# Performance work log

Hardware: AMD Instinct MI355X
Metric: run time of the kernel (lower is better)

The kernel has to match this reference:

```python
import jax, jax.numpy as jnp
import numpy as np

D = 32          # d_lat // 2
D_ANCIL = 16
HID = 128
GRID = 64
N = GRID * GRID # n_patch / n_state
B = 8
DT = 0.25
T_MAX = 4.0
N_STEPS = 18    # enough half/full Strang steps to exceed T_MAX for all batch elems


def _grid_neighbours(g):
    # 4 nearest neighbours on a periodic g x g dual mesh
    idx = np.arange(g * g).reshape(g, g)
    nbrs = np.stack([np.roll(idx, 1, 0), np.roll(idx, -1, 0),
                     np.roll(idx, 1, 1), np.roll(idx, -1, 1)], axis=-1)
    return jnp.asarray(nbrs.reshape(g * g, 4), dtype=jnp.int32)


def setup_inputs() -> dict:
    key = jax.random.key(0)
    ks = jax.random.split(key, 8)
    din = 2 * D + D_ANCIL  # concat(z, neighbour-mean z, xi)
    s1 = 1.0 / np.sqrt(din)
    s2 = 1.0 / np.sqrt(HID)
    return {
        "x": jax.random.normal(ks[0], (B, N, 2 * D + D_ANCIL), jnp.float32),
        "t_final": jax.random.uniform(ks[1], (B,), jnp.float32) * T_MAX,
        "W1_q": jax.random.normal(ks[2], (din, HID), jnp.float32) * s1,
        "b1_q": jnp.zeros((HID,), jnp.float32),
        "W2_q": jax.random.normal(ks[3], (HID, D), jnp.float32) * s2,
        "b2_q": jnp.zeros((D,), jnp.float32),
        "W1_p": jax.random.normal(ks[4], (din, HID), jnp.float32) * s1,
        "b1_p": jnp.zeros((HID,), jnp.float32),
        "W2_p": jax.random.normal(ks[5], (HID, D), jnp.float32) * s2,
        "b2_p": jnp.zeros((D,), jnp.float32),
        "nbrs": _grid_neighbours(GRID),
    }


def _F(z, xi, nbrs, W1, b1, W2, b2):
    # nearest-neighbour forcing: per-node MLP on (z, mean of neighbour z, xi)
    z_nbr = jnp.mean(z[:, nbrs, :], axis=2)           # (B,N,4,D) -> (B,N,D)
    h = jnp.tanh(jnp.concatenate([z, z_nbr, xi], axis=-1) @ W1 + b1)
    return h @ W2 + b2                                 # (B,N,D)


def _masked_stepsize(t, t_final, dt):
    # per-batch stepsize, clipped so integration stops exactly at t_final
    return jnp.clip(t_final - t, 0.0, dt)


def reference(x, t_final, W1_q, b1_q, W2_q, b2_q, W1_p, b1_p, W2_p, b2_p, nbrs):
    q = x[..., :D]
    p = x[..., D:2 * D]
    xi = x[..., 2 * D:]
    tf = t_final[:, None, None]  # broadcast over (N, D)

    def step(carry, k):
        q, p, t_q, t_p = carry
        rho = jnp.where(k == 0, jnp.float32(0.5), jnp.float32(1.0))
        dt_q = _masked_stepsize(t_q, tf, rho * DT)
        q = q + dt_q * _F(p, xi, nbrs, W1_q, b1_q, W2_q, b2_q)
        t_q = t_q + rho * DT
        dt_p = _masked_stepsize(t_p, tf, DT)
        p = p + dt_p * _F(q, xi, nbrs, W1_p, b1_p, W2_p, b2_p)
        t_p = t_p + DT
        return (q, p, t_q, t_p), None

    init = (q, p, jnp.float32(0.0), jnp.float32(0.0))
    (q, p, _, _), _ = jax.lax.scan(step, init, jnp.arange(N_STEPS))
    return jnp.concatenate([q, p, xi], axis=-1)
```

## Files before the change

kernel.cpp:

```cpp
#include <hip/hip_runtime.h>
#include <hip/hip_bf16.h>

#define GRID_W 64
#define NPTS   4096
#define BATCH  8
#define DD     32
#define DIN    80
#define HID    128
#define SH_STRIDE 136
#define SQ_STRIDE 36
#define NBLK   512
#define NSTEP  34
#define OFF_F1Q 131072
#define OFF_F2Q (OFF_F1Q + 24*64*16)
#define OFF_F1P (OFF_F2Q + 8*64*16)
#define OFF_F2P (OFF_F1P + 24*64*16)
#define OFF_EBUF 262144

typedef __attribute__((ext_vector_type(8))) short short8;
typedef __attribute__((ext_vector_type(4))) float f32x4;
typedef unsigned long long u64;

__device__ __forceinline__ ushort f2bf(float v) {
    __hip_bfloat16 h = __float2bfloat16(v);
    return __builtin_bit_cast(ushort, h);
}
__device__ __forceinline__ uint packbf(float a, float b) {
    return (uint)f2bf(a) | ((uint)f2bf(b) << 16);
}
__device__ __forceinline__ short8 pack8(float4 a, float4 b) {
    union { uint u[4]; short8 s; } t;
    t.u[0] = packbf(a.x, a.y); t.u[1] = packbf(a.z, a.w);
    t.u[2] = packbf(b.x, b.y); t.u[3] = packbf(b.z, b.w);
    return t.s;
}
__device__ __forceinline__ float bf2f(ushort u) {
    union { uint i; float f; } t; t.i = ((uint)u) << 16; return t.f;
}

__device__ __forceinline__ short8 ld_sysh8(const ushort* p) {
    union { u64 v[2]; short8 s; } t;
    t.v[0] = __hip_atomic_load((const u64*)p,       __ATOMIC_RELAXED, __HIP_MEMORY_SCOPE_SYSTEM);
    t.v[1] = __hip_atomic_load((const u64*)(p + 4), __ATOMIC_RELAXED, __HIP_MEMORY_SCOPE_SYSTEM);
    return t.s;
}
__device__ __forceinline__ void st_sysb4(ushort* p, float4 v) {
    u64 pk = (u64)packbf(v.x, v.y) | ((u64)packbf(v.z, v.w) << 32);
    __hip_atomic_store((u64*)p, pk, __ATOMIC_RELAXED, __HIP_MEMORY_SCOPE_SYSTEM);
}

__global__ void setup_all(const float* __restrict__ x, float* __restrict__ out,
                          char* __restrict__ ws,
                          const float* __restrict__ W1q, const float* __restrict__ W2q,
                          const float* __restrict__ W1p, const float* __restrict__ W2p)
{
    const int blk = blockIdx.x, tid = threadIdx.x;
    if (blk >= NBLK) {
        const int s = blk - NBLK;
        const float* W1 = s ? W1p : W1q;
        const float* W2 = s ? W2p : W2q;
        ushort* f1 = (ushort*)(ws + (s ? OFF_F1P : OFF_F1Q));
        ushort* f2 = (ushort*)(ws + (s ? OFF_F2P : OFF_F2Q));
        for (int idx = tid; idx < 24 * 512; idx += 256) {
            int f = idx >> 9, rem = idx & 511, lane = rem >> 3, j = rem & 7;
            int ks = f >> 3, nt = f & 7;
            int k = ks * 32 + (lane >> 4) * 8 + j, n = nt * 16 + (lane & 15);
            f1[idx] = f2bf(k < DIN ? W1[k * HID + n] : 0.0f);
        }
        for (int idx = tid; idx < 8 * 512; idx += 256) {
            int f = idx >> 9, rem = idx & 511, lane = rem >> 3, j = rem & 7;
            int ks = f >> 1, nt = f & 1;
            int k = ks * 32 + (lane >> 4) * 8 + j, n = nt * 16 + (lane & 15);
            f2[idx] = f2bf(W2[k * DD + n]);
        }
        return;
    }
    const int b = blk >> 6, r = blk & 63;
    if (tid < 64) ((uint*)ws)[blk * 64 + tid] = 0u;
    const int pt = tid >> 2, j4 = tid & 3;
    {
        const float* src = x   + (size_t)(b * NPTS + r * GRID_W + pt) * DIN + j4 * 20;
        float*       dst = out + (size_t)(b * NPTS + r * GRID_W + pt) * DIN + j4 * 20;
        #pragma unroll
        for (int i = 0; i < 5; ++i)
            *(float4*)(dst + i * 4) = *(const float4*)(src + i * 4);
    }
    {
        const int sg = j4 * 8;
        const float* src = x + (size_t)(b * NPTS + r * GRID_W + pt) * DIN;
        ushort* drow = (ushort*)(ws + OFF_EBUF) + ((size_t)(b * 64 + r) * 64 + pt) * 64;
        float4 q0 = *(const float4*)(src + sg),      q1 = *(const float4*)(src + sg + 4);
        float4 p0 = *(const float4*)(src + DD + sg), p1 = *(const float4*)(src + DD + sg + 4);
        *(uint*)&drow[sg]          = packbf(q0.x, q0.y);
        *(uint*)&drow[sg + 2]      = packbf(q0.z, q0.w);
        *(uint*)&drow[sg + 4]      = packbf(q1.x, q1.y);
        *(uint*)&drow[sg + 6]      = packbf(q1.z, q1.w);
        *(uint*)&drow[32 + sg]     = packbf(p0.x, p0.y);
        *(uint*)&drow[32 + sg + 2] = packbf(p0.z, p0.w);
        *(uint*)&drow[32 + sg + 4] = packbf(p1.x, p1.y);
        *(uint*)&drow[32 + sg + 6] = packbf(p1.z, p1.w);
    }
}

struct Acc2 { f32x4 a0, a1; };

__device__ __forceinline__ Acc2 eval_F(short8 af0, short8 af1, short8 af2,
    const short8* __restrict__ F1, const short8* __restrict__ w2,
    const float* __restrict__ B1, ushort* __restrict__ sH,
    int wv, int lane, int l16, int quad, int q8)
{
    f32x4 acc1[8];
    #pragma unroll
    for (int nt = 0; nt < 8; ++nt) acc1[nt] = (f32x4){0.f, 0.f, 0.f, 0.f};
    #pragma unroll
    for (int nt = 0; nt < 8; ++nt)
        acc1[nt] = __builtin_amdgcn_mfma_f32_16x16x32_bf16(af0, F1[nt * 64 + lane], acc1[nt], 0, 0, 0);
    #pragma unroll
    for (int nt = 0; nt < 8; ++nt)
        acc1[nt] = __builtin_amdgcn_mfma_f32_16x16x32_bf16(af1, F1[(8 + nt) * 64 + lane], acc1[nt], 0, 0, 0);
    #pragma unroll
    for (int nt = 0; nt < 8; ++nt)
        acc1[nt] = __builtin_amdgcn_mfma_f32_16x16x32_bf16(af2, F1[(16 + nt) * 64 + lane], acc1[nt], 0, 0, 0);
    #pragma unroll
    for (int nt = 0; nt < 8; ++nt) {
        const int col = nt * 16 + l16;
        const float bias = B1[col];
        #pragma unroll
        for (int rg = 0; rg < 4; ++rg) {
            const int rowm = wv * 16 + quad * 4 + rg;
            float s = acc1[nt][rg] + bias;
            float e = __expf(2.0f * s);
            float hh = 1.0f - __fdividef(2.0f, e + 1.0f);
            sH[rowm * SH_STRIDE + col] = f2bf(hh);
        }
    }
    Acc2 o;
    o.a0 = (f32x4){0.f, 0.f, 0.f, 0.f};
    o.a1 = (f32x4){0.f, 0.f, 0.f, 0.f};
    #pragma unroll
    for (int ks = 0; ks < 4; ++ks) {
        short8 af = *(const short8*)&sH[(wv * 16 + l16) * SH_STRIDE + ks * 32 + q8];
        o.a0 = __builtin_amdgcn_mfma_f32_16x16x32_bf16(af, w2[ks * 2 + 0], o.a0, 0, 0, 0);
        o.a1 = __builtin_amdgcn_mfma_f32_16x16x32_bf16(af, w2[ks * 2 + 1], o.a1, 0, 0, 0);
    }
    return o;
}

__global__ __launch_bounds__(256, 2) void sympl_coop(
    float* __restrict__ out, const float* __restrict__ tfinal,
    char* __restrict__ ws,
    const float* __restrict__ b1q, const float* __restrict__ b2q,
    const float* __restrict__ b1p, const float* __restrict__ b2p)
{
    __shared__ __align__(16) float  sQ[64 * SQ_STRIDE];
    __shared__ __align__(16) float  sP[64 * SQ_STRIDE];
    __shared__ __align__(16) ushort sH[64 * SH_STRIDE];
    __shared__ __align__(16) float  sO[4 * 512];
    __shared__ uint ldsF[4];

    uint* flags = (uint*)ws;
    ushort* ebuf = (ushort*)(ws + OFF_EBUF);
    const int blk = blockIdx.x, tid = threadIdx.x;
    const int b = blk >> 6, r = blk & 63;
    const int wv = tid >> 6, lane = tid & 63;
    const int l16 = lane & 15, quad = lane >> 4, q8 = quad * 8;
    const int c = wv * 16 + l16;
    const int rm = (r + 63) & 63, rp = (r + 1) & 63;
    const int cm = (c + 63) & 63, cp = (c + 1) & 63;
    const int pt = tid >> 2, sg = (tid & 3) * 8;

    uint* flLw = flags + (((size_t)(b * 64 + rm) * 4) + wv) * 16;
    uint* flRw = flags + (((size_t)(b * 64 + rp) * 4) + wv) * 16;
    uint* flOw = flags + (((size_t)(b * 64 + r ) * 4) + wv) * 16;

    {
        const float* src = out + (size_t)(b * NPTS + r * GRID_W + pt) * DIN;
        *(float4*)&sQ[pt * SQ_STRIDE + sg]     = *(const float4*)(src + sg);
        *(float4*)&sQ[pt * SQ_STRIDE + sg + 4] = *(const float4*)(src + sg + 4);
        *(float4*)&sP[pt * SQ_STRIDE + sg]     = *(const float4*)(src + DD + sg);
        *(float4*)&sP[pt * SQ_STRIDE + sg + 4] = *(const float4*)(src + DD + sg + 4);
    }
    if (tid < 4) ldsF[tid] = 0;
    short8 af2;
    if (quad < 2) {
        const float* px = out + (size_t)(b * NPTS + r * GRID_W + c) * DIN + 2 * DD + q8;
        af2 = pack8(*(const float4*)px, *(const float4*)(px + 4));
    } else {
        af2 = (short8)(short)0;
    }
    short8 w2q[8], w2p[8];
    {
        const short8* F2q = (const short8*)(ws + OFF_F2Q);
        const short8* F2p = (const short8*)(ws + OFF_F2P);
        #pragma unroll
        for (int i = 0; i < 8; ++i) { w2q[i] = F2q[i * 64 + lane]; w2p[i] = F2p[i * 64 + lane]; }
    }
    const float tf = tfinal[b];
    __syncthreads();

    const ushort* e_rm = ebuf + ((size_t)(b * 64 + rm) * 64 + c) * 64;
    const ushort* e_rp = ebuf + ((size_t)(b * 64 + rp) * 64 + c) * 64;
    const int wl = (wv + 3) & 3, wr = (wv + 1) & 3;

    float tq = 0.0f, tp = 0.0f;
    #pragma unroll 1
    for (int h = 0; h < NSTEP; ++h) {
        const int phase = h & 1;
        const float dtmax = phase ? 0.25f : ((h == 0) ? 0.125f : 0.25f);
        const float tcur  = phase ? tp : tq;
        if (!phase && tq >= tf) break;
        if (h > 0) {
            const uint tgt = (uint)h;
            while (true) {
                uint v = tgt;
                if (lane == 0)      v = __hip_atomic_load(flLw, __ATOMIC_RELAXED, __HIP_MEMORY_SCOPE_SYSTEM);
                else if (lane == 1) v = __hip_atomic_load(flRw, __ATOMIC_RELAXED, __HIP_MEMORY_SCOPE_SYSTEM);
                else if (lane == 2) v = __hip_atomic_load(&ldsF[wl], __ATOMIC_RELAXED, __HIP_MEMORY_SCOPE_WORKGROUP);
                else if (lane == 3) v = __hip_atomic_load(&ldsF[wr], __ATOMIC_RELAXED, __HIP_MEMORY_SCOPE_WORKGROUP);
                if (__all((int)(v >= tgt))) break;
                __builtin_amdgcn_s_sleep(1);
            }
        }

        const float dt = fminf(fmaxf(tf - tcur, 0.0f), dtmax);
        if (dt > 0.0f) {
            const int so  = phase ? 0 : 32;
            const int dso = phase ? 32 : 0;
            const float* srcL = phase ? sQ : sP;
            float*       dstL = phase ? sP : sQ;

            short8 upv = ld_sysh8(e_rm + so + q8);
            short8 dnv = ld_sysh8(e_rp + so + q8);

            const float* s0p = srcL + c * SQ_STRIDE + q8;
            float4 a0 = *(const float4*)s0p, a1 = *(const float4*)(s0p + 4);
            short8 af0 = pack8(a0, a1);

            const short8* F1 = (const short8*)(ws + (phase ? OFF_F1P : OFF_F1Q));
            f32x4 acc1[8];
            #pragma unroll
            for (int nt = 0; nt < 8; ++nt) acc1[nt] = (f32x4){0.f, 0.f, 0.f, 0.f};
            #pragma unroll
            for (int nt = 0; nt < 8; ++nt)
                acc1[nt] = __builtin_amdgcn_mfma_f32_16x16x32_bf16(af0, F1[nt * 64 + lane], acc1[nt], 0, 0, 0);
            #pragma unroll
            for (int nt = 0; nt < 8; ++nt)
                acc1[nt] = __builtin_amdgcn_mfma_f32_16x16x32_bf16(af2, F1[(16 + nt) * 64 + lane], acc1[nt], 0, 0, 0);

            const float* smp = srcL + cm * SQ_STRIDE + q8;
            const float* spp = srcL + cp * SQ_STRIDE + q8;
            float4 lf0 = *(const float4*)smp, lf1 = *(const float4*)(smp + 4);
            float4 rt0 = *(const float4*)spp, rt1 = *(const float4*)(spp + 4);
            float4 m0, m1;
            m0.x = 0.25f * (bf2f((ushort)upv[0]) + bf2f((ushort)dnv[0]) + lf0.x + rt0.x);
            m0.y = 0.25f * (bf2f((ushort)upv[1]) + bf2f((ushort)dnv[1]) + lf0.y + rt0.y);
            m0.z = 0.25f * (bf2f((ushort)upv[2]) + bf2f((ushort)dnv[2]) + lf0.z + rt0.z);
            m0.w = 0.25f * (bf2f((ushort)upv[3]) + bf2f((ushort)dnv[3]) + lf0.w + rt0.w);
            m1.x = 0.25f * (bf2f((ushort)upv[4]) + bf2f((ushort)dnv[4]) + lf1.x + rt1.x);
            m1.y = 0.25f * (bf2f((ushort)upv[5]) + bf2f((ushort)dnv[5]) + lf1.y + rt1.y);
            m1.z = 0.25f * (bf2f((ushort)upv[6]) + bf2f((ushort)dnv[6]) + lf1.z + rt1.z);
            m1.w = 0.25f * (bf2f((ushort)upv[7]) + bf2f((ushort)dnv[7]) + lf1.w + rt1.w);
            short8 af1 = pack8(m0, m1);
            #pragma unroll
            for (int nt = 0; nt < 8; ++nt)
                acc1[nt] = __builtin_amdgcn_mfma_f32_16x16x32_bf16(af1, F1[(8 + nt) * 64 + lane], acc1[nt], 0, 0, 0);

            const float* B1 = phase ? b1p : b1q;
            #pragma unroll
            for (int nt = 0; nt < 8; ++nt) {
                const int col = nt * 16 + l16;
                const float bias = B1[col];
                #pragma unroll
                for (int rg = 0; rg < 4; ++rg) {
                    const int rowm = wv * 16 + quad * 4 + rg;
                    float s = acc1[nt][rg] + bias;
                    float e = __expf(2.0f * s);
                    float hh = 1.0f - __fdividef(2.0f, e + 1.0f);
                    sH[rowm * SH_STRIDE + col] = f2bf(hh);
                }
            }
            const short8* w2 = phase ? w2p : w2q;
            f32x4 o0 = (f32x4){0.f, 0.f, 0.f, 0.f};
            f32x4 o1 = (f32x4){0.f, 0.f, 0.f, 0.f};
            #pragma unroll
            for (int ks = 0; ks < 4; ++ks) {
                short8 af = *(const short8*)&sH[(wv * 16 + l16) * SH_STRIDE + ks * 32 + q8];
                o0 = __builtin_amdgcn_mfma_f32_16x16x32_bf16(af, w2[ks * 2 + 0], o0, 0, 0, 0);
                o1 = __builtin_amdgcn_mfma_f32_16x16x32_bf16(af, w2[ks * 2 + 1], o1, 0, 0, 0);
            }
            float* sOw = sO + wv * 512;
            const float* B2 = phase ? b2p : b2q;
            #pragma unroll
            for (int nt = 0; nt < 2; ++nt) {
                const int col = nt * 16 + l16;
                const float b2v = B2[col];
                const f32x4 av = nt ? o1 : o0;
                #pragma unroll
                for (int rg = 0; rg < 4; ++rg)
                    sOw[(quad * 4 + rg) * DD + col] = av[rg] + b2v;
            }
            #pragma unroll
            for (int it = 0; it < 2; ++it) {
                const int slot = lane + it * 64;
                const int lr = slot >> 3, seg = (slot & 7) * 4;
                const int pt_ = wv * 16 + lr;
                const float* po = &sOw[lr * DD + seg];
                float* pl = dstL + pt_ * SQ_STRIDE + seg;
                float4 o = *(const float4*)pl;
                o.x += dt * po[0]; o.y += dt * po[1];
                o.z += dt * po[2]; o.w += dt * po[3];
                st_sysb4(ebuf + ((size_t)(b * 64 + r) * 64 + pt_) * 64 + dso + seg, o);
                *(float4*)pl = o;
            }
        }
        __asm__ volatile("s_waitcnt vmcnt(0)" ::: "memory");
        if (lane == 0)
            __hip_atomic_store(flOw, (uint)(h + 1), __ATOMIC_RELAXED, __HIP_MEMORY_SCOPE_SYSTEM);
        __asm__ volatile("s_waitcnt lgkmcnt(0)" ::: "memory");
        if (lane == 0)
            __hip_atomic_store(&ldsF[wv], (uint)(h + 1), __ATOMIC_RELAXED, __HIP_MEMORY_SCOPE_WORKGROUP);
        if (phase) tp += dtmax; else tq += dtmax;
    }

    {
        float* dst = out + (size_t)(b * NPTS + r * GRID_W + pt) * DIN;
        *(float4*)(dst + sg)          = *(const float4*)&sQ[pt * SQ_STRIDE + sg];
        *(float4*)(dst + sg + 4)      = *(const float4*)&sQ[pt * SQ_STRIDE + sg + 4];
        *(float4*)(dst + DD + sg)     = *(const float4*)&sP[pt * SQ_STRIDE + sg];
        *(float4*)(dst + DD + sg + 4) = *(const float4*)&sP[pt * SQ_STRIDE + sg + 4];
    }
}

__global__ __launch_bounds__(256, 2) void sympl_step(
    float* __restrict__ state, const float* __restrict__ tfinal,
    const char* __restrict__ ws,
    const float* __restrict__ B1, const float* __restrict__ B2,
    int phase, float tcur, float dtmax)
{
    __shared__ __align__(16) ushort sH[64 * SH_STRIDE];
    __shared__ __align__(16) float  sO[4 * 512];
    const int blk = blockIdx.x, tid = threadIdx.x;
    const int wv = tid >> 6, lane = tid & 63;
    const int l16 = lane & 15, quad = lane >> 4, q8 = quad * 8;
    const int b = blk >> 6, r = blk & 63;
    const int c = wv * 16 + l16;

    const float tf = tfinal[b];
    const float dt = fminf(fmaxf(tf - tcur, 0.0f), dtmax);
    if (dt <= 0.0f) return;

    const int srcoff = phase ? 0 : DD;
    const int dstoff = phase ? DD : 0;
    float* bb = state + (size_t)b * NPTS * DIN;
    const float* selfp = bb + (r * GRID_W + c) * DIN;
    const int rm = (r + 63) & 63, rp = (r + 1) & 63;
    const int cm = (c + 63) & 63, cp = (c + 1) & 63;
    short8 af0, af1, af2;
    {
        const float* ps = selfp + srcoff + q8;
        af0 = pack8(*(const float4*)ps, *(const float4*)(ps + 4));
    }
    {
        const float* p0 = bb + (rm * GRID_W + c) * DIN + srcoff + q8;
        const float* p1 = bb + (rp * GRID_W + c) * DIN + srcoff + q8;
        const float* p2 = bb + (r * GRID_W + cm) * DIN + srcoff + q8;
        const float* p3 = bb + (r * GRID_W + cp) * DIN + srcoff + q8;
        float4 a0 = *(const float4*)p0, a1 = *(const float4*)(p0 + 4);
        float4 b0 = *(const float4*)p1, b1v = *(const float4*)(p1 + 4);
        float4 c0 = *(const float4*)p2, c1 = *(const float4*)(p2 + 4);
        float4 d0 = *(const float4*)p3, d1 = *(const float4*)(p3 + 4);
        float4 m0, m1;
        m0.x = 0.25f * (a0.x + b0.x + c0.x + d0.x);
        m0.y = 0.25f * (a0.y + b0.y + c0.y + d0.y);
        m0.z = 0.25f * (a0.z + b0.z + c0.z + d0.z);
        m0.w = 0.25f * (a0.w + b0.w + c0.w + d0.w);
        m1.x = 0.25f * (a1.x + b1v.x + c1.x + d1.x);
        m1.y = 0.25f * (a1.y + b1v.y + c1.y + d1.y);
        m1.z = 0.25f * (a1.z + b1v.z + c1.z + d1.z);
        m1.w = 0.25f * (a1.w + b1v.w + c1.w + d1.w);
        af1 = pack8(m0, m1);
    }
    if (quad < 2) {
        const float* px = selfp + 2 * DD + q8;
        af2 = pack8(*(const float4*)px, *(const float4*)(px + 4));
    } else {
        af2 = (short8)(short)0;
    }
    const short8* F1 = (const short8*)(ws + (phase ? OFF_F1P : OFF_F1Q));
    const short8* F2 = (const short8*)(ws + (phase ? OFF_F2P : OFF_F2Q));
    short8 w2[8];
    #pragma unroll
    for (int i = 0; i < 8; ++i) w2[i] = F2[i * 64 + lane];
    Acc2 A = eval_F(af0, af1, af2, F1, w2, B1, sH, wv, lane, l16, quad, q8);
    float* sOw = sO + wv * 512;
    #pragma unroll
    for (int nt = 0; nt < 2; ++nt) {
        const int col = nt * 16 + l16;
        const float b2v = B2[col];
        const f32x4 av = nt ? A.a1 : A.a0;
        #pragma unroll
        for (int rg = 0; rg < 4; ++rg)
            sOw[(quad * 4 + rg) * DD + col] = av[rg] + b2v;
    }
    #pragma unroll
    for (int it = 0; it < 2; ++it) {
        const int slot = lane + it * 64;
        const int lr = slot >> 3, seg = (slot & 7) * 4;
        float* pd = bb + (r * GRID_W + wv * 16 + lr) * DIN + dstoff + seg;
        const float* po = &sOw[lr * DD + seg];
        float4 o = *(const float4*)pd;
        o.x += dt * po[0]; o.y += dt * po[1];
        o.z += dt * po[2]; o.w += dt * po[3];
        *(float4*)pd = o;
    }
}

extern "C" void kernel_launch(void* const* d_in, const int* in_sizes, int n_in,
                              void* d_out, int out_size, void* d_ws, size_t ws_size,
                              hipStream_t stream)
{
    const float* x   = (const float*)d_in[0];
    const float* tf  = (const float*)d_in[1];
    const float* W1q = (const float*)d_in[2];
    const float* b1q = (const float*)d_in[3];
    const float* W2q = (const float*)d_in[4];
    const float* b2q = (const float*)d_in[5];
    const float* W1p = (const float*)d_in[6];
    const float* b1p = (const float*)d_in[7];
    const float* W2p = (const float*)d_in[8];
    const float* b2p = (const float*)d_in[9];
    float* out = (float*)d_out;
    char* ws = (char*)d_ws;

    setup_all<<<dim3(NBLK + 2), dim3(256), 0, stream>>>(x, out, ws, W1q, W2q, W1p, W2p);

    void* args[] = { (void*)&out, (void*)&tf, (void*)&ws,
                     (void*)&b1q, (void*)&b2q, (void*)&b1p, (void*)&b2p };
    hipError_t e = hipLaunchCooperativeKernel((const void*)sympl_coop,
                                              dim3(NBLK), dim3(256), args, 0, stream);
    if (e != hipSuccess) {
        float tq = 0.0f, tp = 0.0f;
        for (int h = 0; h < NSTEP; ++h) {
            const int phase = h & 1;
            const float dtmax = phase ? 0.25f : ((h == 0) ? 0.125f : 0.25f);
            const float tcur  = phase ? tp : tq;
            sympl_step<<<dim3(NBLK), dim3(256), 0, stream>>>(
                out, tf, ws, phase ? b1p : b1q, phase ? b2p : b2q,
                phase, tcur, dtmax);
            if (phase) tp += dtmax; else tq += dtmax;
        }
    }
}
```

Baseline: 250.0 us.

## Embed step tags in halo data words and overlap first GEMM with neighbour wait

Replaces the separate per-wave flag counters with a 16-bit step tag packed into the top of every 64-bit halo word (three bf16 values plus tag), so consumers poll the data itself rather than a flag followed by a data load. The self-and-xi part of the first GEMM is moved ahead of the neighbour wait so it can overlap with the synchronisation latency. This removes the vmcnt drain and flag store on the producer side. In exchange the halo buffer grows, each consumer spins on six system-scope loads, and a workspace-size check is added before using the cooperative path.

```diff
diff --git a/kernel.cpp b/kernel.cpp
--- a/kernel.cpp
+++ b/kernel.cpp
@@ -16,6 +16,8 @@
 #define OFF_F1P (OFF_F2Q + 8*64*16)
 #define OFF_F2P (OFF_F1P + 24*64*16)
 #define OFF_EBUF 262144
+#define EB_U64_TOTAL ((size_t)NBLK * 64 * 24)
+#define WS_NEED ((size_t)OFF_EBUF + EB_U64_TOTAL * 8)
 
 typedef __attribute__((ext_vector_type(8))) short short8;
 typedef __attribute__((ext_vector_type(4))) float f32x4;
@@ -38,21 +40,18 @@
     union { uint i; float f; } t; t.i = ((uint)u) << 16; return t.f;
 }
 
-__device__ __forceinline__ short8 ld_sysh8(const ushort* p) {
-    union { u64 v[2]; short8 s; } t;
-    t.v[0] = __hip_atomic_load((const u64*)p,       __ATOMIC_RELAXED, __HIP_MEMORY_SCOPE_SYSTEM);
-    t.v[1] = __hip_atomic_load((const u64*)(p + 4), __ATOMIC_RELAXED, __HIP_MEMORY_SCOPE_SYSTEM);
-    return t.s;
-}
-__device__ __forceinline__ void st_sysb4(ushort* p, float4 v) {
-    u64 pk = (u64)packbf(v.x, v.y) | ((u64)packbf(v.z, v.w) << 32);
-    __hip_atomic_store((u64*)p, pk, __ATOMIC_RELAXED, __HIP_MEMORY_SCOPE_SYSTEM);
+__device__ __forceinline__ u64 ld_sys64(const u64* p) {
+    return __hip_atomic_load(p, __ATOMIC_RELAXED, __HIP_MEMORY_SCOPE_SYSTEM);
+}
+__device__ __forceinline__ void st_sys64(u64* p, u64 v) {
+    __hip_atomic_store(p, v, __ATOMIC_RELAXED, __HIP_MEMORY_SCOPE_SYSTEM);
 }
 
 __global__ void setup_all(const float* __restrict__ x, float* __restrict__ out,
                           char* __restrict__ ws,
                           const float* __restrict__ W1q, const float* __restrict__ W2q,
-                          const float* __restrict__ W1p, const float* __restrict__ W2p)
+                          const float* __restrict__ W1p, const float* __restrict__ W2p,
+                          int do_ebuf)
 {
     const int blk = blockIdx.x, tid = threadIdx.x;
     if (blk >= NBLK) {
@@ -76,29 +75,30 @@
         return;
     }
     const int b = blk >> 6, r = blk & 63;
-    if (tid < 64) ((uint*)ws)[blk * 64 + tid] = 0u;
     const int pt = tid >> 2, j4 = tid & 3;
-    {
-        const float* src = x   + (size_t)(b * NPTS + r * GRID_W + pt) * DIN + j4 * 20;
-        float*       dst = out + (size_t)(b * NPTS + r * GRID_W + pt) * DIN + j4 * 20;
+    const float* src = x + (size_t)(b * NPTS + r * GRID_W + pt) * DIN;
+    {
+        float* dst = out + (size_t)(b * NPTS + r * GRID_W + pt) * DIN + j4 * 20;
+        const float* s4 = src + j4 * 20;
         #pragma unroll
         for (int i = 0; i < 5; ++i)
-            *(float4*)(dst + i * 4) = *(const float4*)(src + i * 4);
-    }
-    {
-        const int sg = j4 * 8;
-        const float* src = x + (size_t)(b * NPTS + r * GRID_W + pt) * DIN;
-        ushort* drow = (ushort*)(ws + OFF_EBUF) + ((size_t)(b * 64 + r) * 64 + pt) * 64;
-        float4 q0 = *(const float4*)(src + sg),      q1 = *(const float4*)(src + sg + 4);
-        float4 p0 = *(const float4*)(src + DD + sg), p1 = *(const float4*)(src + DD + sg + 4);
-        *(uint*)&drow[sg]          = packbf(q0.x, q0.y);
-        *(uint*)&drow[sg + 2]      = packbf(q0.z, q0.w);
-        *(uint*)&drow[sg + 4]      = packbf(q1.x, q1.y);
-        *(uint*)&drow[sg + 6]      = packbf(q1.z, q1.w);
-        *(uint*)&drow[32 + sg]     = packbf(p0.x, p0.y);
-        *(uint*)&drow[32 + sg + 2] = packbf(p0.z, p0.w);
-        *(uint*)&drow[32 + sg + 4] = packbf(p1.x, p1.y);
-        *(uint*)&drow[32 + sg + 6] = packbf(p1.z, p1.w);
+            *(float4*)(dst + i * 4) = *(const float4*)(s4 + i * 4);
+    }
+    if (do_ebuf) {
+        u64* drow = (u64*)(ws + OFF_EBUF) + ((size_t)((b * 64 + r) * 64) + pt) * 24;
+        #pragma unroll
+        for (int k = 0; k < 6; ++k) {
+            const int m = j4 * 6 + k;
+            const int half = m / 12, sub = m % 12;
+            const int qR = sub / 3, u = sub - qR * 3;
+            const int sbase = qR * 8 + u * 3, cap = qR * 8 + 7;
+            const int i1 = (sbase + 1 > cap) ? cap : sbase + 1;
+            const int i2 = (sbase + 2 > cap) ? cap : sbase + 2;
+            const float* hs = src + (half ? DD : 0);
+            u64 pk = (u64)f2bf(hs[sbase]) | ((u64)f2bf(hs[i1]) << 16)
+                   | ((u64)f2bf(hs[i2]) << 32);
+            drow[half * 12 + qR * 3 + u] = pk;
+        }
     }
 }
 
@@ -158,8 +158,7 @@
     __shared__ __align__(16) float  sO[4 * 512];
     __shared__ uint ldsF[4];
 
-    uint* flags = (uint*)ws;
-    ushort* ebuf = (ushort*)(ws + OFF_EBUF);
+    u64* eb = (u64*)(ws + OFF_EBUF);
     const int blk = blockIdx.x, tid = threadIdx.x;
     const int b = blk >> 6, r = blk & 63;
     const int wv = tid >> 6, lane = tid & 63;
@@ -169,9 +168,11 @@
     const int cm = (c + 63) & 63, cp = (c + 1) & 63;
     const int pt = tid >> 2, sg = (tid & 3) * 8;
 
-    uint* flLw = flags + (((size_t)(b * 64 + rm) * 4) + wv) * 16;
-    uint* flRw = flags + (((size_t)(b * 64 + rp) * 4) + wv) * 16;
-    uint* flOw = flags + (((size_t)(b * 64 + r ) * 4) + wv) * 16;
+    const u64* prm = eb + ((size_t)(b * 64 + rm) * 64 + c) * 24 + quad * 3;
+    const u64* prp = eb + ((size_t)(b * 64 + rp) * 64 + c) * 24 + quad * 3;
+    const u64* s_rm = eb + ((size_t)(b * 64 + rm) * 64 + (wv * 16 + 15)) * 24 + 11;
+    const u64* s_rp = eb + ((size_t)(b * 64 + rp) * 64 + (wv * 16 + 15)) * 24 + 11;
+    u64* pub = eb + ((size_t)(b * 64 + r) * 64) * 24;
 
     {
         const float* src = out + (size_t)(b * NPTS + r * GRID_W + pt) * DIN;
@@ -198,8 +199,6 @@
     const float tf = tfinal[b];
     __syncthreads();
 
-    const ushort* e_rm = ebuf + ((size_t)(b * 64 + rm) * 64 + c) * 64;
-    const ushort* e_rp = ebuf + ((size_t)(b * 64 + rp) * 64 + c) * 64;
     const int wl = (wv + 3) & 3, wr = (wv + 1) & 3;
 
     float tq = 0.0f, tp = 0.0f;
@@ -209,35 +208,19 @@
         const float dtmax = phase ? 0.25f : ((h == 0) ? 0.125f : 0.25f);
         const float tcur  = phase ? tp : tq;
         if (!phase && tq >= tf) break;
-        if (h > 0) {
-            const uint tgt = (uint)h;
-            while (true) {
-                uint v = tgt;
-                if (lane == 0)      v = __hip_atomic_load(flLw, __ATOMIC_RELAXED, __HIP_MEMORY_SCOPE_SYSTEM);
-                else if (lane == 1) v = __hip_atomic_load(flRw, __ATOMIC_RELAXED, __HIP_MEMORY_SCOPE_SYSTEM);
-                else if (lane == 2) v = __hip_atomic_load(&ldsF[wl], __ATOMIC_RELAXED, __HIP_MEMORY_SCOPE_WORKGROUP);
-                else if (lane == 3) v = __hip_atomic_load(&ldsF[wr], __ATOMIC_RELAXED, __HIP_MEMORY_SCOPE_WORKGROUP);
-                if (__all((int)(v >= tgt))) break;
-                __builtin_amdgcn_s_sleep(1);
-            }
-        }
-
         const float dt = fminf(fmaxf(tf - tcur, 0.0f), dtmax);
+        const int srcH = phase ^ 1;
+        const int dstH = phase;
+        const float* srcL = phase ? sQ : sP;
+        float*       dstL = phase ? sP : sQ;
+        const short8* F1 = (const short8*)(ws + (phase ? OFF_F1P : OFF_F1Q));
+        const uint hh = (uint)h;
+
+        f32x4 acc1[8];
         if (dt > 0.0f) {
-            const int so  = phase ? 0 : 32;
-            const int dso = phase ? 32 : 0;
-            const float* srcL = phase ? sQ : sP;
-            float*       dstL = phase ? sP : sQ;
-
-            short8 upv = ld_sysh8(e_rm + so + q8);
-            short8 dnv = ld_sysh8(e_rp + so + q8);
-
             const float* s0p = srcL + c * SQ_STRIDE + q8;
             float4 a0 = *(const float4*)s0p, a1 = *(const float4*)(s0p + 4);
             short8 af0 = pack8(a0, a1);
-
-            const short8* F1 = (const short8*)(ws + (phase ? OFF_F1P : OFF_F1Q));
-            f32x4 acc1[8];
             #pragma unroll
             for (int nt = 0; nt < 8; ++nt) acc1[nt] = (f32x4){0.f, 0.f, 0.f, 0.f};
             #pragma unroll
@@ -246,20 +229,45 @@
             #pragma unroll
             for (int nt = 0; nt < 8; ++nt)
                 acc1[nt] = __builtin_amdgcn_mfma_f32_16x16x32_bf16(af2, F1[(16 + nt) * 64 + lane], acc1[nt], 0, 0, 0);
+        }
+
+        while (true) {
+            bool ok = true;
+            if (lane == 0)      ok = ((uint)(ld_sys64(s_rm + srcH * 12) >> 48) == hh);
+            else if (lane == 1) ok = ((uint)(ld_sys64(s_rp + srcH * 12) >> 48) == hh);
+            else if (lane == 2) ok = (__hip_atomic_load(&ldsF[wl], __ATOMIC_RELAXED, __HIP_MEMORY_SCOPE_WORKGROUP) >= hh);
+            else if (lane == 3) ok = (__hip_atomic_load(&ldsF[wr], __ATOMIC_RELAXED, __HIP_MEMORY_SCOPE_WORKGROUP) >= hh);
+            if (__all((int)ok)) break;
+            __builtin_amdgcn_s_sleep(1);
+        }
+
+        if (dt > 0.0f) {
+            const u64* pA = prm + srcH * 12;
+            const u64* pB = prp + srcH * 12;
+            u64 a0, a1, a2, c0, c1, c2;
+            while (true) {
+                a0 = ld_sys64(pA);     a1 = ld_sys64(pA + 1); a2 = ld_sys64(pA + 2);
+                c0 = ld_sys64(pB);     c1 = ld_sys64(pB + 1); c2 = ld_sys64(pB + 2);
+                bool ok = ((uint)(a0 >> 48) == hh) & ((uint)(a1 >> 48) == hh)
+                        & ((uint)(a2 >> 48) == hh) & ((uint)(c0 >> 48) == hh)
+                        & ((uint)(c1 >> 48) == hh) & ((uint)(c2 >> 48) == hh);
+                if (__all((int)ok)) break;
+                __builtin_amdgcn_s_sleep(1);
+            }
 
             const float* smp = srcL + cm * SQ_STRIDE + q8;
             const float* spp = srcL + cp * SQ_STRIDE + q8;
             float4 lf0 = *(const float4*)smp, lf1 = *(const float4*)(smp + 4);
             float4 rt0 = *(const float4*)spp, rt1 = *(const float4*)(spp + 4);
             float4 m0, m1;
-            m0.x = 0.25f * (bf2f((ushort)upv[0]) + bf2f((ushort)dnv[0]) + lf0.x + rt0.x);
-            m0.y = 0.25f * (bf2f((ushort)upv[1]) + bf2f((ushort)dnv[1]) + lf0.y + rt0.y);
-            m0.z = 0.25f * (bf2f((ushort)upv[2]) + bf2f((ushort)dnv[2]) + lf0.z + rt0.z);
-            m0.w = 0.25f * (bf2f((ushort)upv[3]) + bf2f((ushort)dnv[3]) + lf0.w + rt0.w);
-            m1.x = 0.25f * (bf2f((ushort)upv[4]) + bf2f((ushort)dnv[4]) + lf1.x + rt1.x);
-            m1.y = 0.25f * (bf2f((ushort)upv[5]) + bf2f((ushort)dnv[5]) + lf1.y + rt1.y);
-            m1.z = 0.25f * (bf2f((ushort)upv[6]) + bf2f((ushort)dnv[6]) + lf1.z + rt1.z);
-            m1.w = 0.25f * (bf2f((ushort)upv[7]) + bf2f((ushort)dnv[7]) + lf1.w + rt1.w);
+            m0.x = 0.25f * (bf2f((ushort)a0)         + bf2f((ushort)c0)         + lf0.x + rt0.x);
+            m0.y = 0.25f * (bf2f((ushort)(a0 >> 16)) + bf2f((ushort)(c0 >> 16)) + lf0.y + rt0.y);
+            m0.z = 0.25f * (bf2f((ushort)(a0 >> 32)) + bf2f((ushort)(c0 >> 32)) + lf0.z + rt0.z);
+            m0.w = 0.25f * (bf2f((ushort)a1)         + bf2f((ushort)c1)         + lf0.w + rt0.w);
+            m1.x = 0.25f * (bf2f((ushort)(a1 >> 16)) + bf2f((ushort)(c1 >> 16)) + lf1.x + rt1.x);
+            m1.y = 0.25f * (bf2f((ushort)(a1 >> 32)) + bf2f((ushort)(c1 >> 32)) + lf1.y + rt1.y);
+            m1.z = 0.25f * (bf2f((ushort)a2)         + bf2f((ushort)c2)         + lf1.z + rt1.z);
+            m1.w = 0.25f * (bf2f((ushort)(a2 >> 16)) + bf2f((ushort)(c2 >> 16)) + lf1.w + rt1.w);
             short8 af1 = pack8(m0, m1);
             #pragma unroll
             for (int nt = 0; nt < 8; ++nt)
@@ -275,8 +283,8 @@
                     const int rowm = wv * 16 + quad * 4 + rg;
                     float s = acc1[nt][rg] + bias;
                     float e = __expf(2.0f * s);
-                    float hh = 1.0f - __fdividef(2.0f, e + 1.0f);
-                    sH[rowm * SH_STRIDE + col] = f2bf(hh);
+                    float hhv = 1.0f - __fdividef(2.0f, e + 1.0f);
+                    sH[rowm * SH_STRIDE + col] = f2bf(hhv);
                 }
             }
             const short8* w2 = phase ? w2p : w2q;
@@ -309,13 +317,23 @@
                 float4 o = *(const float4*)pl;
                 o.x += dt * po[0]; o.y += dt * po[1];
                 o.z += dt * po[2]; o.w += dt * po[3];
-                st_sysb4(ebuf + ((size_t)(b * 64 + r) * 64 + pt_) * 64 + dso + seg, o);
                 *(float4*)pl = o;
             }
-        }
-        __asm__ volatile("s_waitcnt vmcnt(0)" ::: "memory");
-        if (lane == 0)
-            __hip_atomic_store(flOw, (uint)(h + 1), __ATOMIC_RELAXED, __HIP_MEMORY_SCOPE_SYSTEM);
+            const u64 tg = ((u64)(ushort)(hh + 1)) << 48;
+            #pragma unroll
+            for (int t = 0; t < 3; ++t) {
+                const int g = t * 64 + lane;
+                const int pt_ = g / 12, sub = g - pt_ * 12;
+                const int qR = sub / 3, u = sub - qR * 3;
+                const int sbase = qR * 8 + u * 3, cap = qR * 8 + 7;
+                const int i1 = (sbase + 1 > cap) ? cap : sbase + 1;
+                const int i2 = (sbase + 2 > cap) ? cap : sbase + 2;
+                const float* pd = dstL + (wv * 16 + pt_) * SQ_STRIDE;
+                u64 pk = (u64)f2bf(pd[sbase]) | ((u64)f2bf(pd[i1]) << 16)
+                       | ((u64)f2bf(pd[i2]) << 32) | tg;
+                st_sys64(pub + (size_t)(wv * 16 + pt_) * 24 + dstH * 12 + qR * 3 + u, pk);
+            }
+        }
         __asm__ volatile("s_waitcnt lgkmcnt(0)" ::: "memory");
         if (lane == 0)
             __hip_atomic_store(&ldsF[wv], (uint)(h + 1), __ATOMIC_RELAXED, __HIP_MEMORY_SCOPE_WORKGROUP);
@@ -432,12 +450,18 @@
     float* out = (float*)d_out;
     char* ws = (char*)d_ws;
 
-    setup_all<<<dim3(NBLK + 2), dim3(256), 0, stream>>>(x, out, ws, W1q, W2q, W1p, W2p);
-
-    void* args[] = { (void*)&out, (void*)&tf, (void*)&ws,
-                     (void*)&b1q, (void*)&b2q, (void*)&b1p, (void*)&b2p };
-    hipError_t e = hipLaunchCooperativeKernel((const void*)sympl_coop,
-                                              dim3(NBLK), dim3(256), args, 0, stream);
+    const int coop_ok = (ws_size >= WS_NEED) ? 1 : 0;
+
+    setup_all<<<dim3(NBLK + 2), dim3(256), 0, stream>>>(x, out, ws, W1q, W2q,
+                                                        W1p, W2p, coop_ok);
+
+    hipError_t e = hipErrorUnknown;
+    if (coop_ok) {
+        void* args[] = { (void*)&out, (void*)&tf, (void*)&ws,
+                         (void*)&b1q, (void*)&b2q, (void*)&b1p, (void*)&b2p };
+        e = hipLaunchCooperativeKernel((const void*)sympl_coop,
+                                       dim3(NBLK), dim3(256), args, 0, stream);
+    }
     if (e != hipSuccess) {
         float tq = 0.0f, tp = 0.0f;
         for (int h = 0; h < NSTEP; ++h) {
```

Result: no change. 253.2 us (+1.3%).
